# Kernel tuning notes

Hardware: AMD Instinct MI355X
Metric: run time of the kernel (lower is better)

## Reference

```python
import jax, jax.numpy as jnp
import numpy as np

N_NODES = 50000
IN_CH = 128
HID = 128
OUT_CH = 40
N_LAYERS = 3
N_EDGES = 600000


def setup_inputs() -> dict:
    key = jax.random.key(0)
    ks = jax.random.split(key, 4 + 5 * N_LAYERS)
    x = jax.random.normal(ks[0], (N_NODES, IN_CH), dtype=jnp.float32)
    edge_attr = jax.random.normal(ks[1], (N_EDGES, 4), dtype=jnp.float32)
    edge_index = jax.random.randint(ks[2], (2, N_EDGES), 0, N_NODES, dtype=jnp.int64)
    # Per-layer MLP params ([in->hid->hid]); in==hid so stack as [L, d, d].
    def glorot(k, fan_in, fan_out):
        s = jnp.sqrt(2.0 / (fan_in + fan_out)).astype(jnp.float32)
        return jax.random.normal(k, (fan_in, fan_out), dtype=jnp.float32) * s
    W1 = jnp.stack([glorot(ks[3 + i], IN_CH if i == 0 else HID, HID) for i in range(N_LAYERS)])
    b1 = jnp.zeros((N_LAYERS, HID), dtype=jnp.float32)
    W2 = jnp.stack([glorot(ks[3 + N_LAYERS + i], HID, HID) for i in range(N_LAYERS)])
    b2 = jnp.zeros((N_LAYERS, HID), dtype=jnp.float32)
    Wc = glorot(ks[3 + 2 * N_LAYERS], HID, OUT_CH)
    bc = jnp.zeros((OUT_CH,), dtype=jnp.float32)
    return {"x": x, "edge_attr": edge_attr, "edge_index": edge_index,
            "W1": W1, "b1": b1, "W2": W2, "b2": b2, "Wc": Wc, "bc": bc}


def reference(x, edge_attr, edge_index, W1, b1, W2, b2, Wc, bc):
    # GIN node classifier, eval mode (dropout = identity, BN = identity).
    src, dst = edge_index[0], edge_index[1]
    h = x
    for i in range(N_LAYERS):
        # GINConv (eps=0): aggregate sum of neighbor features via scatter-add.
        msgs = h[src]                                   # [E, d] gather
        aggr = jax.ops.segment_sum(msgs, dst, num_segments=N_NODES)  # [N, d]
        z = h + aggr                                    # (1+eps)*x + sum
        z = jax.nn.relu(z @ W1[i] + b1[i])              # MLP hidden
        z = z @ W2[i] + b2[i]                           # MLP out
        h = jax.nn.relu(z)                              # F.relu(conv(...))
    return h @ Wc + bc                                  # [N, OUT_CH]
```

## Files before the change

### kernel.cpp

```cpp
#include <hip/hip_runtime.h>

#define N_NODES 50000
#define IN_CH 128
#define HID 128
#define OUT_CH 40
#define N_LAYERS 3
#define N_EDGES 600000
#define DSTRIDE 64
#define DEGSTRIDE 32

typedef __attribute__((ext_vector_type(8))) short short8;
typedef __attribute__((ext_vector_type(4))) float floatx4;

static __device__ __forceinline__ unsigned short f32_to_bf16(float f) {
  unsigned u = __float_as_uint(f);
  unsigned r = 0x7FFFu + ((u >> 16) & 1u);
  return (unsigned short)((u + r) >> 16);
}
static __device__ __forceinline__ float bf16_to_f32(unsigned short h) {
  return __uint_as_float(((unsigned)h) << 16);
}

#define CONV_BLOCKS 6250
#define W_BLOCKS 408
#define DEG_BLOCKS 1563

__global__ __launch_bounds__(256) void prep_all_kernel(
    const float* __restrict__ x, const float* __restrict__ W1,
    const float* __restrict__ W2, const float* __restrict__ Wc,
    unsigned short* __restrict__ xb, unsigned short* __restrict__ WT,
    unsigned short* __restrict__ WcT, unsigned short* __restrict__ hb1,
    int* __restrict__ deg) {
  const int b = blockIdx.x;
  const int t = threadIdx.x;
  if (b < CONV_BLOCKS) {
    int i = (b * 256 + t) * 4;
    if (i < N_NODES * 128) {
      float4 v = *(const float4*)(x + i);
      ushort4 o;
      o.x = f32_to_bf16(v.x); o.y = f32_to_bf16(v.y);
      o.z = f32_to_bf16(v.z); o.w = f32_to_bf16(v.w);
      *(ushort4*)(xb + i) = o;
    }
  } else if (b < CONV_BLOCKS + W_BLOCKS) {
    int o = (b - CONV_BLOCKS) * 256 + t;
    if (o < 6 * 16384) {
      int mat = o >> 14;
      int r = o & 16383;
      int n = r >> 7;
      int k = r & 127;
      const float* W = (mat < 3) ? (W1 + (size_t)mat * 16384)
                                 : (W2 + (size_t)(mat - 3) * 16384);
      WT[(size_t)mat * 16384 + (size_t)n * 128 + k] =
          f32_to_bf16(W[(size_t)k * 128 + n]);
    } else if (o < 6 * 16384 + 48 * 128) {
      int r = o - 6 * 16384;
      int n = r >> 7;
      int k = r & 127;
      float v = (n < OUT_CH) ? Wc[(size_t)k * OUT_CH + n] : 0.0f;
      WcT[(size_t)n * 128 + k] = f32_to_bf16(v);
    }
  } else if (b < CONV_BLOCKS + W_BLOCKS + DEG_BLOCKS) {
    int i = ((b - CONV_BLOCKS - W_BLOCKS) * 256 + t) * 4;
    if (i < N_NODES * DEGSTRIDE) *(int4*)(deg + i) = make_int4(0, 0, 0, 0);
  } else {
    if (t < 128) xb[(size_t)N_NODES * 128 + t] = 0;
    else hb1[(size_t)N_NODES * 128 + (t - 128)] = 0;
  }
}

#define CSR_BLOCKS 586
__global__ __launch_bounds__(256) void csr_kernel(
    const int* __restrict__ ei, int* __restrict__ deg, int* __restrict__ col) {
  int base = (blockIdx.x * 256 + threadIdx.x) * 4;
  if (base >= N_EDGES) return;
  int4 s4 = *(const int4*)(ei + base);
  int4 d4 = *(const int4*)(ei + N_EDGES + base);
  int p0 = atomicAdd(&deg[(size_t)d4.x * DEGSTRIDE], 1);
  int p1 = atomicAdd(&deg[(size_t)d4.y * DEGSTRIDE], 1);
  int p2 = atomicAdd(&deg[(size_t)d4.z * DEGSTRIDE], 1);
  int p3 = atomicAdd(&deg[(size_t)d4.w * DEGSTRIDE], 1);
  col[(size_t)d4.x * DSTRIDE + p0] = s4.x;
  col[(size_t)d4.y * DSTRIDE + p1] = s4.y;
  col[(size_t)d4.z * DSTRIDE + p2] = s4.z;
  col[(size_t)d4.w * DSTRIDE + p3] = s4.w;
}

__global__ __launch_bounds__(256) void aggregate_kernel(
    const unsigned short* __restrict__ h, const int* __restrict__ deg,
    const int* __restrict__ col, unsigned short* __restrict__ z) {
  int n = __builtin_amdgcn_readfirstlane(blockIdx.x * 4 + (threadIdx.x >> 6));
  int q = threadIdx.x & 63;
  const size_t co = (size_t)q * 2;
  ushort2 sv = *(const ushort2*)(h + (size_t)n * 128 + co);
  float ax[8], ay[8];
#pragma unroll
  for (int k = 0; k < 8; ++k) { ax[k] = 0.f; ay[k] = 0.f; }
  ax[0] = bf16_to_f32(sv.x);
  ay[0] = bf16_to_f32(sv.y);
  int dg = __builtin_amdgcn_readfirstlane(deg[(size_t)n * DEGSTRIDE]);
  int cnt = (dg + 15) & ~15;
  const int* cp = col + (size_t)n * DSTRIDE;
  for (int i = 0; i < cnt; i += 16) {
    int ss[16];
#pragma unroll
    for (int k = 0; k < 16; ++k) {
      int sl = cp[i + k];
      ss[k] = __builtin_amdgcn_readfirstlane((i + k < dg) ? sl : N_NODES);
    }
    ushort2 vv[16];
#pragma unroll
    for (int k = 0; k < 16; ++k)
      vv[k] = *(const ushort2*)(h + (size_t)ss[k] * 128 + co);
#pragma unroll
    for (int k = 0; k < 16; ++k) {
      ax[k & 7] += bf16_to_f32(vv[k].x);
      ay[k & 7] += bf16_to_f32(vv[k].y);
    }
  }
  float s0 = (ax[0] + ax[1]) + (ax[2] + ax[3]) + (ax[4] + ax[5]) + (ax[6] + ax[7]);
  float s1 = (ay[0] + ay[1]) + (ay[2] + ay[3]) + (ay[4] + ay[5]) + (ay[6] + ay[7]);
  ushort2 o;
  o.x = f32_to_bf16(s0);
  o.y = f32_to_bf16(s1);
  *(ushort2*)(z + (size_t)n * 128 + co) = o;
}

template <bool LAST>
__global__ __launch_bounds__(256) void layer_pair_kernel(
    const unsigned short* __restrict__ A, const unsigned short* __restrict__ WT1,
    const float* __restrict__ b1, const unsigned short* __restrict__ WT2,
    const float* __restrict__ b2, unsigned short* __restrict__ Z,
    const unsigned short* __restrict__ WcT, const float* __restrict__ bc,
    float* __restrict__ out, int M) {
  __shared__ __align__(16) unsigned short Wl[128][136];
  __shared__ __align__(16) unsigned short T[64][136];
  const int tid = threadIdx.x;
  const int w = tid >> 6;
  const int lane = tid & 63;
  const int qg = lane >> 4;
  const int ln = lane & 15;
  const int row0 = blockIdx.x * 64;
  const int rbase = w * 16;
  const int r0 = row0 + rbase + ln;
  const short8 zero8 = {0, 0, 0, 0, 0, 0, 0, 0};

#pragma unroll
  for (int j = 0; j < 8; ++j) {
    int slot = tid + j * 256;
    int row = slot >> 4;
    int kb = slot & 15;
    *(short8*)&Wl[row][kb * 8] = *(const short8*)(WT1 + (size_t)row * 128 + kb * 8);
  }
  __syncthreads();

  floatx4 acc[8];
#pragma unroll
  for (int ct = 0; ct < 8; ++ct) acc[ct] = (floatx4){0.f, 0.f, 0.f, 0.f};
#pragma unroll
  for (int ks = 0; ks < 4; ++ks) {
    const int koff = ks * 32 + qg * 8;
    short8 a = (r0 < M) ? *(const short8*)(A + (size_t)r0 * 128 + koff) : zero8;
#pragma unroll
    for (int ct = 0; ct < 8; ++ct) {
      short8 b = *(const short8*)&Wl[ct * 16 + ln][koff];
      acc[ct] = __builtin_amdgcn_mfma_f32_16x16x32_bf16(a, b, acc[ct], 0, 0, 0);
    }
  }
#pragma unroll
  for (int ct = 0; ct < 8; ++ct) {
    float bv = b1[ct * 16 + ln];
#pragma unroll
    for (int r = 0; r < 4; ++r) {
      float v = fmaxf(acc[ct][r] + bv, 0.0f);
      T[rbase + qg * 4 + r][ct * 16 + ln] = f32_to_bf16(v);
    }
  }

  __syncthreads();
#pragma unroll
  for (int j = 0; j < 8; ++j) {
    int slot = tid + j * 256;
    int row = slot >> 4;
    int kb = slot & 15;
    *(short8*)&Wl[row][kb * 8] = *(const short8*)(WT2 + (size_t)row * 128 + kb * 8);
  }
  __syncthreads();

  floatx4 acc2[8];
#pragma unroll
  for (int ct = 0; ct < 8; ++ct) acc2[ct] = (floatx4){0.f, 0.f, 0.f, 0.f};
#pragma unroll
  for (int ks = 0; ks < 4; ++ks) {
    const int koff = ks * 32 + qg * 8;
    short8 a = *(const short8*)&T[rbase + ln][koff];
#pragma unroll
    for (int ct = 0; ct < 8; ++ct) {
      short8 b = *(const short8*)&Wl[ct * 16 + ln][koff];
      acc2[ct] = __builtin_amdgcn_mfma_f32_16x16x32_bf16(a, b, acc2[ct], 0, 0, 0);
    }
  }
#pragma unroll
  for (int ct = 0; ct < 8; ++ct) {
    float bv = b2[ct * 16 + ln];
#pragma unroll
    for (int r = 0; r < 4; ++r) {
      float v = fmaxf(acc2[ct][r] + bv, 0.0f);
      T[rbase + qg * 4 + r][ct * 16 + ln] = f32_to_bf16(v);
    }
  }

  if (LAST) {
    floatx4 acc3[3];
#pragma unroll
    for (int ct = 0; ct < 3; ++ct) acc3[ct] = (floatx4){0.f, 0.f, 0.f, 0.f};
#pragma unroll
    for (int ks = 0; ks < 4; ++ks) {
      const int koff = ks * 32 + qg * 8;
      short8 a = *(const short8*)&T[rbase + ln][koff];
#pragma unroll
      for (int ct = 0; ct < 3; ++ct) {
        short8 b = *(const short8*)(WcT + (size_t)(ct * 16 + ln) * 128 + koff);
        acc3[ct] = __builtin_amdgcn_mfma_f32_16x16x32_bf16(a, b, acc3[ct], 0, 0, 0);
      }
    }
#pragma unroll
    for (int ct = 0; ct < 3; ++ct) {
      int colg = ct * 16 + ln;
      if (colg < OUT_CH) {
        float bv = bc[colg];
#pragma unroll
        for (int r = 0; r < 4; ++r) {
          int row = row0 + rbase + qg * 4 + r;
          if (row < M) out[(size_t)row * OUT_CH + colg] = acc3[ct][r] + bv;
        }
      }
    }
  } else {
    __syncthreads();
#pragma unroll
    for (int j = 0; j < 4; ++j) {
      int slot = tid + j * 256;
      int row = slot >> 4;
      int kb = slot & 15;
      if (row0 + row < M) {
        short8 v = *(const short8*)&T[row][kb * 8];
        *(short8*)(Z + (size_t)(row0 + row) * 128 + kb * 8) = v;
      }
    }
  }
}

extern "C" void kernel_launch(void* const* d_in, const int* in_sizes, int n_in,
                              void* d_out, int out_size, void* d_ws,
                              size_t ws_size, hipStream_t stream) {
  const float* x = (const float*)d_in[0];
  const int* ei = (const int*)d_in[2];
  const float* W1 = (const float*)d_in[3];
  const float* b1 = (const float*)d_in[4];
  const float* W2 = (const float*)d_in[5];
  const float* b2 = (const float*)d_in[6];
  const float* Wc = (const float*)d_in[7];
  const float* bc = (const float*)d_in[8];
  float* out = (float*)d_out;

  const size_t NF = (size_t)(N_NODES + 1) * 128;
  unsigned short* hb0 = (unsigned short*)d_ws;
  unsigned short* hb1 = hb0 + NF;
  unsigned short* xbf = hb1 + NF;
  unsigned short* WT = xbf + NF;
  unsigned short* WcT = WT + 6 * 16384;
  int* deg = (int*)(WcT + 48 * 128);
  int* col = deg + (size_t)N_NODES * DEGSTRIDE;

  const dim3 blk(256);
  const int aggr_grid = N_NODES / 4;
  const int pair_grid = (N_NODES + 63) / 64;

  prep_all_kernel<<<CONV_BLOCKS + W_BLOCKS + DEG_BLOCKS + 1, blk, 0, stream>>>(
      x, W1, W2, Wc, xbf, WT, WcT, hb1, deg);

  csr_kernel<<<CSR_BLOCKS, blk, 0, stream>>>(ei, deg, col);

  const unsigned short* h = xbf;
  for (int l = 0; l < N_LAYERS; ++l) {
    aggregate_kernel<<<aggr_grid, blk, 0, stream>>>(h, deg, col, hb0);
    if (l < N_LAYERS - 1) {
      layer_pair_kernel<false><<<pair_grid, blk, 0, stream>>>(
          hb0, WT + (size_t)l * 16384, b1 + (size_t)l * 128,
          WT + (size_t)(3 + l) * 16384, b2 + (size_t)l * 128, hb1,
          nullptr, nullptr, nullptr, N_NODES);
      h = hb1;
    } else {
      layer_pair_kernel<true><<<pair_grid, blk, 0, stream>>>(
          hb0, WT + (size_t)l * 16384, b1 + (size_t)l * 128,
          WT + (size_t)(3 + l) * 16384, b2 + (size_t)l * 128, nullptr,
          WcT, bc, out, N_NODES);
    }
  }
}
```

Before: 245.5 us.

## Gather neighbor rows with 16-byte loads split across lane groups in aggregation

The aggregation kernel now has each wavefront split into four 16-lane groups. Each group loads a whole neighbor row with 16-byte short8 loads, handling four neighbors per step, and the partial sums are combined with cross-lane shuffles. Previously every lane did a 4-byte load per neighbor, so this cuts the number of memory instructions per gathered row at the cost of extra shuffles and idle lanes in the final store. The CSR build kernel also changes from four edges per thread with int4 loads to one edge per thread with a larger grid.

```diff
diff --git a/kernel.cpp b/kernel.cpp
--- a/kernel.cpp
+++ b/kernel.cpp
@@ -69,61 +69,61 @@
   }
 }
 
-#define CSR_BLOCKS 586
 __global__ __launch_bounds__(256) void csr_kernel(
     const int* __restrict__ ei, int* __restrict__ deg, int* __restrict__ col) {
-  int base = (blockIdx.x * 256 + threadIdx.x) * 4;
-  if (base >= N_EDGES) return;
-  int4 s4 = *(const int4*)(ei + base);
-  int4 d4 = *(const int4*)(ei + N_EDGES + base);
-  int p0 = atomicAdd(&deg[(size_t)d4.x * DEGSTRIDE], 1);
-  int p1 = atomicAdd(&deg[(size_t)d4.y * DEGSTRIDE], 1);
-  int p2 = atomicAdd(&deg[(size_t)d4.z * DEGSTRIDE], 1);
-  int p3 = atomicAdd(&deg[(size_t)d4.w * DEGSTRIDE], 1);
-  col[(size_t)d4.x * DSTRIDE + p0] = s4.x;
-  col[(size_t)d4.y * DSTRIDE + p1] = s4.y;
-  col[(size_t)d4.z * DSTRIDE + p2] = s4.z;
-  col[(size_t)d4.w * DSTRIDE + p3] = s4.w;
+  int e = blockIdx.x * 256 + threadIdx.x;
+  if (e >= N_EDGES) return;
+  int s = ei[e];
+  int d = ei[N_EDGES + e];
+  int pos = atomicAdd(&deg[(size_t)d * DEGSTRIDE], 1);
+  col[(size_t)d * DSTRIDE + pos] = s;
 }
 
 __global__ __launch_bounds__(256) void aggregate_kernel(
     const unsigned short* __restrict__ h, const int* __restrict__ deg,
     const int* __restrict__ col, unsigned short* __restrict__ z) {
   int n = __builtin_amdgcn_readfirstlane(blockIdx.x * 4 + (threadIdx.x >> 6));
-  int q = threadIdx.x & 63;
-  const size_t co = (size_t)q * 2;
-  ushort2 sv = *(const ushort2*)(h + (size_t)n * 128 + co);
-  float ax[8], ay[8];
-#pragma unroll
-  for (int k = 0; k < 8; ++k) { ax[k] = 0.f; ay[k] = 0.f; }
-  ax[0] = bf16_to_f32(sv.x);
-  ay[0] = bf16_to_f32(sv.y);
+  const int lane = threadIdx.x & 63;
+  const int g = lane >> 4;
+  const int p = lane & 15;
+  short8 sv = *(const short8*)(h + (size_t)n * 128 + p * 8);
+  float acc[8];
+#pragma unroll
+  for (int j = 0; j < 8; ++j)
+    acc[j] = (g == 0) ? bf16_to_f32((unsigned short)sv[j]) : 0.f;
+
   int dg = __builtin_amdgcn_readfirstlane(deg[(size_t)n * DEGSTRIDE]);
   int cnt = (dg + 15) & ~15;
   const int* cp = col + (size_t)n * DSTRIDE;
   for (int i = 0; i < cnt; i += 16) {
-    int ss[16];
-#pragma unroll
-    for (int k = 0; k < 16; ++k) {
-      int sl = cp[i + k];
-      ss[k] = __builtin_amdgcn_readfirstlane((i + k < dg) ? sl : N_NODES);
-    }
-    ushort2 vv[16];
-#pragma unroll
-    for (int k = 0; k < 16; ++k)
-      vv[k] = *(const ushort2*)(h + (size_t)ss[k] * 128 + co);
-#pragma unroll
-    for (int k = 0; k < 16; ++k) {
-      ax[k & 7] += bf16_to_f32(vv[k].x);
-      ay[k & 7] += bf16_to_f32(vv[k].y);
-    }
-  }
-  float s0 = (ax[0] + ax[1]) + (ax[2] + ax[3]) + (ax[4] + ax[5]) + (ax[6] + ax[7]);
-  float s1 = (ay[0] + ay[1]) + (ay[2] + ay[3]) + (ay[4] + ay[5]) + (ay[6] + ay[7]);
-  ushort2 o;
-  o.x = f32_to_bf16(s0);
-  o.y = f32_to_bf16(s1);
-  *(ushort2*)(z + (size_t)n * 128 + co) = o;
+    short8 v[4];
+#pragma unroll
+    for (int b = 0; b < 4; ++b) {
+      int r = i + b * 4;
+      int s0 = __builtin_amdgcn_readfirstlane((r + 0 < dg) ? cp[r + 0] : N_NODES);
+      int s1 = __builtin_amdgcn_readfirstlane((r + 1 < dg) ? cp[r + 1] : N_NODES);
+      int s2 = __builtin_amdgcn_readfirstlane((r + 2 < dg) ? cp[r + 2] : N_NODES);
+      int s3 = __builtin_amdgcn_readfirstlane((r + 3 < dg) ? cp[r + 3] : N_NODES);
+      int myrow = (g == 1) ? s1 : (g == 2) ? s2 : (g == 3) ? s3 : s0;
+      v[b] = *(const short8*)(h + (size_t)myrow * 128 + p * 8);
+    }
+#pragma unroll
+    for (int b = 0; b < 4; ++b)
+#pragma unroll
+      for (int j = 0; j < 8; ++j)
+        acc[j] += bf16_to_f32((unsigned short)v[b][j]);
+  }
+#pragma unroll
+  for (int j = 0; j < 8; ++j) {
+    acc[j] += __shfl_xor(acc[j], 16, 64);
+    acc[j] += __shfl_xor(acc[j], 32, 64);
+  }
+  if (g == 0) {
+    short8 o;
+#pragma unroll
+    for (int j = 0; j < 8; ++j) o[j] = (short)f32_to_bf16(acc[j]);
+    *(short8*)(z + (size_t)n * 128 + p * 8) = o;
+  }
 }
 
 template <bool LAST>
@@ -274,13 +274,14 @@
   int* col = deg + (size_t)N_NODES * DEGSTRIDE;
 
   const dim3 blk(256);
+  const int edge_grid = (N_EDGES + 255) / 256;
   const int aggr_grid = N_NODES / 4;
   const int pair_grid = (N_NODES + 63) / 64;
 
   prep_all_kernel<<<CONV_BLOCKS + W_BLOCKS + DEG_BLOCKS + 1, blk, 0, stream>>>(
       x, W1, W2, Wc, xbf, WT, WcT, hb1, deg);
 
-  csr_kernel<<<CSR_BLOCKS, blk, 0, stream>>>(ei, deg, col);
+  csr_kernel<<<edge_grid, blk, 0, stream>>>(ei, deg, col);
 
   const unsigned short* h = xbf;
   for (int l = 0; l < N_LAYERS; ++l) {
```

New measurement: 255.6 us. 4.1% more time.

## Replace padded per-node CSR with atomicExch linked lists for edge adjacency

Applied to the files above, without the earlier changes.

Builds per-destination adjacency as singly linked lists using atomicExch on a head array, and stores (src,next) pairs per edge instead of writing into fixed 64-slot padded rows. The aggregation kernel walks two node lists per wavefront in an interleaved loop, so each wave processes two nodes. This shrinks the adjacency memory and the zeroing work, and removes the degree cap of 64. The cost is a serial pointer-chasing dependency per edge, which replaces the previous 16-wide batched index loads and adds latency on every hop.

```diff
diff --git a/kernel.cpp b/kernel.cpp
--- a/kernel.cpp
+++ b/kernel.cpp
@@ -6,8 +6,7 @@
 #define OUT_CH 40
 #define N_LAYERS 3
 #define N_EDGES 600000
-#define DSTRIDE 64
-#define DEGSTRIDE 32
+#define HEADSTRIDE 16
 
 typedef __attribute__((ext_vector_type(8))) short short8;
 typedef __attribute__((ext_vector_type(4))) float floatx4;
@@ -23,14 +22,14 @@
 
 #define CONV_BLOCKS 6250
 #define W_BLOCKS 408
-#define DEG_BLOCKS 1563
+#define HEAD_BLOCKS 782
 
 __global__ __launch_bounds__(256) void prep_all_kernel(
     const float* __restrict__ x, const float* __restrict__ W1,
     const float* __restrict__ W2, const float* __restrict__ Wc,
     unsigned short* __restrict__ xb, unsigned short* __restrict__ WT,
     unsigned short* __restrict__ WcT, unsigned short* __restrict__ hb1,
-    int* __restrict__ deg) {
+    int* __restrict__ head) {
   const int b = blockIdx.x;
   const int t = threadIdx.x;
   if (b < CONV_BLOCKS) {
@@ -60,9 +59,10 @@
       float v = (n < OUT_CH) ? Wc[(size_t)k * OUT_CH + n] : 0.0f;
       WcT[(size_t)n * 128 + k] = f32_to_bf16(v);
     }
-  } else if (b < CONV_BLOCKS + W_BLOCKS + DEG_BLOCKS) {
+  } else if (b < CONV_BLOCKS + W_BLOCKS + HEAD_BLOCKS) {
     int i = ((b - CONV_BLOCKS - W_BLOCKS) * 256 + t) * 4;
-    if (i < N_NODES * DEGSTRIDE) *(int4*)(deg + i) = make_int4(0, 0, 0, 0);
+    if (i < N_NODES * HEADSTRIDE)
+      *(int4*)(head + i) = make_int4(-1, -1, -1, -1);
   } else {
     if (t < 128) xb[(size_t)N_NODES * 128 + t] = 0;
     else hb1[(size_t)N_NODES * 128 + (t - 128)] = 0;
@@ -71,59 +71,57 @@
 
 #define CSR_BLOCKS 586
 __global__ __launch_bounds__(256) void csr_kernel(
-    const int* __restrict__ ei, int* __restrict__ deg, int* __restrict__ col) {
+    const int* __restrict__ ei, int* __restrict__ head, int* __restrict__ lst) {
   int base = (blockIdx.x * 256 + threadIdx.x) * 4;
   if (base >= N_EDGES) return;
   int4 s4 = *(const int4*)(ei + base);
   int4 d4 = *(const int4*)(ei + N_EDGES + base);
-  int p0 = atomicAdd(&deg[(size_t)d4.x * DEGSTRIDE], 1);
-  int p1 = atomicAdd(&deg[(size_t)d4.y * DEGSTRIDE], 1);
-  int p2 = atomicAdd(&deg[(size_t)d4.z * DEGSTRIDE], 1);
-  int p3 = atomicAdd(&deg[(size_t)d4.w * DEGSTRIDE], 1);
-  col[(size_t)d4.x * DSTRIDE + p0] = s4.x;
-  col[(size_t)d4.y * DSTRIDE + p1] = s4.y;
-  col[(size_t)d4.z * DSTRIDE + p2] = s4.z;
-  col[(size_t)d4.w * DSTRIDE + p3] = s4.w;
+  int n0 = atomicExch(&head[(size_t)d4.x * HEADSTRIDE], base + 0);
+  int n1 = atomicExch(&head[(size_t)d4.y * HEADSTRIDE], base + 1);
+  int n2 = atomicExch(&head[(size_t)d4.z * HEADSTRIDE], base + 2);
+  int n3 = atomicExch(&head[(size_t)d4.w * HEADSTRIDE], base + 3);
+  *(int4*)(lst + 2 * (size_t)base) = make_int4(s4.x, n0, s4.y, n1);
+  *(int4*)(lst + 2 * (size_t)base + 4) = make_int4(s4.z, n2, s4.w, n3);
 }
 
 __global__ __launch_bounds__(256) void aggregate_kernel(
-    const unsigned short* __restrict__ h, const int* __restrict__ deg,
-    const int* __restrict__ col, unsigned short* __restrict__ z) {
-  int n = __builtin_amdgcn_readfirstlane(blockIdx.x * 4 + (threadIdx.x >> 6));
-  int q = threadIdx.x & 63;
+    const unsigned short* __restrict__ h, const int* __restrict__ head,
+    const int* __restrict__ lst, unsigned short* __restrict__ z) {
+  const int w = threadIdx.x >> 6;
+  int n0 = __builtin_amdgcn_readfirstlane(blockIdx.x * 8 + w * 2);
+  int n1 = n0 + 1;
+  const int q = threadIdx.x & 63;
   const size_t co = (size_t)q * 2;
-  ushort2 sv = *(const ushort2*)(h + (size_t)n * 128 + co);
-  float ax[8], ay[8];
-#pragma unroll
-  for (int k = 0; k < 8; ++k) { ax[k] = 0.f; ay[k] = 0.f; }
-  ax[0] = bf16_to_f32(sv.x);
-  ay[0] = bf16_to_f32(sv.y);
-  int dg = __builtin_amdgcn_readfirstlane(deg[(size_t)n * DEGSTRIDE]);
-  int cnt = (dg + 15) & ~15;
-  const int* cp = col + (size_t)n * DSTRIDE;
-  for (int i = 0; i < cnt; i += 16) {
-    int ss[16];
-#pragma unroll
-    for (int k = 0; k < 16; ++k) {
-      int sl = cp[i + k];
-      ss[k] = __builtin_amdgcn_readfirstlane((i + k < dg) ? sl : N_NODES);
-    }
-    ushort2 vv[16];
-#pragma unroll
-    for (int k = 0; k < 16; ++k)
-      vv[k] = *(const ushort2*)(h + (size_t)ss[k] * 128 + co);
-#pragma unroll
-    for (int k = 0; k < 16; ++k) {
-      ax[k & 7] += bf16_to_f32(vv[k].x);
-      ay[k & 7] += bf16_to_f32(vv[k].y);
-    }
-  }
-  float s0 = (ax[0] + ax[1]) + (ax[2] + ax[3]) + (ax[4] + ax[5]) + (ax[6] + ax[7]);
-  float s1 = (ay[0] + ay[1]) + (ay[2] + ay[3]) + (ay[4] + ay[5]) + (ay[6] + ay[7]);
-  ushort2 o;
-  o.x = f32_to_bf16(s0);
-  o.y = f32_to_bf16(s1);
-  *(ushort2*)(z + (size_t)n * 128 + co) = o;
+  ushort2 sv0 = *(const ushort2*)(h + (size_t)n0 * 128 + co);
+  ushort2 sv1 = *(const ushort2*)(h + (size_t)n1 * 128 + co);
+  float a0x = bf16_to_f32(sv0.x), a0y = bf16_to_f32(sv0.y);
+  float a1x = bf16_to_f32(sv1.x), a1y = bf16_to_f32(sv1.y);
+  int e0 = __builtin_amdgcn_readfirstlane(head[(size_t)n0 * HEADSTRIDE]);
+  int e1 = __builtin_amdgcn_readfirstlane(head[(size_t)n1 * HEADSTRIDE]);
+  while (e0 != -1 || e1 != -1) {
+    int s0 = N_NODES, nx0 = -1, s1 = N_NODES, nx1 = -1;
+    if (e0 != -1) {
+      int2 p = *(const int2*)(lst + 2 * (size_t)e0);
+      s0 = p.x; nx0 = p.y;
+    }
+    if (e1 != -1) {
+      int2 p = *(const int2*)(lst + 2 * (size_t)e1);
+      s1 = p.x; nx1 = p.y;
+    }
+    s0 = __builtin_amdgcn_readfirstlane(s0);
+    s1 = __builtin_amdgcn_readfirstlane(s1);
+    ushort2 v0 = *(const ushort2*)(h + (size_t)s0 * 128 + co);
+    ushort2 v1 = *(const ushort2*)(h + (size_t)s1 * 128 + co);
+    a0x += bf16_to_f32(v0.x); a0y += bf16_to_f32(v0.y);
+    a1x += bf16_to_f32(v1.x); a1y += bf16_to_f32(v1.y);
+    e0 = __builtin_amdgcn_readfirstlane(nx0);
+    e1 = __builtin_amdgcn_readfirstlane(nx1);
+  }
+  ushort2 o0, o1;
+  o0.x = f32_to_bf16(a0x); o0.y = f32_to_bf16(a0y);
+  o1.x = f32_to_bf16(a1x); o1.y = f32_to_bf16(a1y);
+  *(ushort2*)(z + (size_t)n0 * 128 + co) = o0;
+  *(ushort2*)(z + (size_t)n1 * 128 + co) = o1;
 }
 
 template <bool LAST>
@@ -270,21 +268,21 @@
   unsigned short* xbf = hb1 + NF;
   unsigned short* WT = xbf + NF;
   unsigned short* WcT = WT + 6 * 16384;
-  int* deg = (int*)(WcT + 48 * 128);
-  int* col = deg + (size_t)N_NODES * DEGSTRIDE;
+  int* head = (int*)(WcT + 48 * 128);
+  int* lst = head + (size_t)N_NODES * HEADSTRIDE;
 
   const dim3 blk(256);
-  const int aggr_grid = N_NODES / 4;
+  const int aggr_grid = N_NODES / 8;
   const int pair_grid = (N_NODES + 63) / 64;
 
-  prep_all_kernel<<<CONV_BLOCKS + W_BLOCKS + DEG_BLOCKS + 1, blk, 0, stream>>>(
-      x, W1, W2, Wc, xbf, WT, WcT, hb1, deg);
-
-  csr_kernel<<<CSR_BLOCKS, blk, 0, stream>>>(ei, deg, col);
+  prep_all_kernel<<<CONV_BLOCKS + W_BLOCKS + HEAD_BLOCKS + 1, blk, 0, stream>>>(
+      x, W1, W2, Wc, xbf, WT, WcT, hb1, head);
+
+  csr_kernel<<<CSR_BLOCKS, blk, 0, stream>>>(ei, head, lst);
 
   const unsigned short* h = xbf;
   for (int l = 0; l < N_LAYERS; ++l) {
-    aggregate_kernel<<<aggr_grid, blk, 0, stream>>>(h, deg, col, hb0);
+    aggregate_kernel<<<aggr_grid, blk, 0, stream>>>(h, head, lst, hb0);
     if (l < N_LAYERS - 1) {
       layer_pair_kernel<false><<<pair_grid, blk, 0, stream>>>(
           hb0, WT + (size_t)l * 16384, b1 + (size_t)l * 128,
```

Result: slower. 332.0 us (+35.3%).

## Fuse neighbor aggregation into per-layer MLP kernel via shared-memory tile

Applied to the files above, without the earlier changes.

Moves the gather-sum aggregation into the layer MLP kernel: each wave aggregates its 16 nodes directly into the LDS tile T, which then feeds the first MFMA GEMM. This removes three aggregate launches and the global round trip of the aggregated features. In exchange, aggregation parallelism drops from 12500 blocks with one node per wave to 782 blocks with 16 serial nodes per wave, which may expose gather latency and lower occupancy. The CSR build is also changed to one edge per thread, and both hidden buffers now get a zero padding row.

```diff
diff --git a/kernel.cpp b/kernel.cpp
--- a/kernel.cpp
+++ b/kernel.cpp
@@ -29,8 +29,8 @@
     const float* __restrict__ x, const float* __restrict__ W1,
     const float* __restrict__ W2, const float* __restrict__ Wc,
     unsigned short* __restrict__ xb, unsigned short* __restrict__ WT,
-    unsigned short* __restrict__ WcT, unsigned short* __restrict__ hb1,
-    int* __restrict__ deg) {
+    unsigned short* __restrict__ WcT, unsigned short* __restrict__ hb0,
+    unsigned short* __restrict__ hb1, int* __restrict__ deg) {
   const int b = blockIdx.x;
   const int t = threadIdx.x;
   if (b < CONV_BLOCKS) {
@@ -64,75 +64,33 @@
     int i = ((b - CONV_BLOCKS - W_BLOCKS) * 256 + t) * 4;
     if (i < N_NODES * DEGSTRIDE) *(int4*)(deg + i) = make_int4(0, 0, 0, 0);
   } else {
-    if (t < 128) xb[(size_t)N_NODES * 128 + t] = 0;
-    else hb1[(size_t)N_NODES * 128 + (t - 128)] = 0;
-  }
-}
-
-#define CSR_BLOCKS 586
+    if (t < 128) {
+      xb[(size_t)N_NODES * 128 + t] = 0;
+      hb0[(size_t)N_NODES * 128 + t] = 0;
+    } else {
+      hb1[(size_t)N_NODES * 128 + (t - 128)] = 0;
+    }
+  }
+}
+
 __global__ __launch_bounds__(256) void csr_kernel(
     const int* __restrict__ ei, int* __restrict__ deg, int* __restrict__ col) {
-  int base = (blockIdx.x * 256 + threadIdx.x) * 4;
-  if (base >= N_EDGES) return;
-  int4 s4 = *(const int4*)(ei + base);
-  int4 d4 = *(const int4*)(ei + N_EDGES + base);
-  int p0 = atomicAdd(&deg[(size_t)d4.x * DEGSTRIDE], 1);
-  int p1 = atomicAdd(&deg[(size_t)d4.y * DEGSTRIDE], 1);
-  int p2 = atomicAdd(&deg[(size_t)d4.z * DEGSTRIDE], 1);
-  int p3 = atomicAdd(&deg[(size_t)d4.w * DEGSTRIDE], 1);
-  col[(size_t)d4.x * DSTRIDE + p0] = s4.x;
-  col[(size_t)d4.y * DSTRIDE + p1] = s4.y;
-  col[(size_t)d4.z * DSTRIDE + p2] = s4.z;
-  col[(size_t)d4.w * DSTRIDE + p3] = s4.w;
-}
-
-__global__ __launch_bounds__(256) void aggregate_kernel(
+  int e = blockIdx.x * 256 + threadIdx.x;
+  if (e >= N_EDGES) return;
+  int s = ei[e];
+  int d = ei[N_EDGES + e];
+  int pos = atomicAdd(&deg[(size_t)d * DEGSTRIDE], 1);
+  col[(size_t)d * DSTRIDE + pos] = s;
+}
+
+template <bool LAST>
+__global__ __launch_bounds__(256) void fused_layer_kernel(
     const unsigned short* __restrict__ h, const int* __restrict__ deg,
-    const int* __restrict__ col, unsigned short* __restrict__ z) {
-  int n = __builtin_amdgcn_readfirstlane(blockIdx.x * 4 + (threadIdx.x >> 6));
-  int q = threadIdx.x & 63;
-  const size_t co = (size_t)q * 2;
-  ushort2 sv = *(const ushort2*)(h + (size_t)n * 128 + co);
-  float ax[8], ay[8];
-#pragma unroll
-  for (int k = 0; k < 8; ++k) { ax[k] = 0.f; ay[k] = 0.f; }
-  ax[0] = bf16_to_f32(sv.x);
-  ay[0] = bf16_to_f32(sv.y);
-  int dg = __builtin_amdgcn_readfirstlane(deg[(size_t)n * DEGSTRIDE]);
-  int cnt = (dg + 15) & ~15;
-  const int* cp = col + (size_t)n * DSTRIDE;
-  for (int i = 0; i < cnt; i += 16) {
-    int ss[16];
-#pragma unroll
-    for (int k = 0; k < 16; ++k) {
-      int sl = cp[i + k];
-      ss[k] = __builtin_amdgcn_readfirstlane((i + k < dg) ? sl : N_NODES);
-    }
-    ushort2 vv[16];
-#pragma unroll
-    for (int k = 0; k < 16; ++k)
-      vv[k] = *(const ushort2*)(h + (size_t)ss[k] * 128 + co);
-#pragma unroll
-    for (int k = 0; k < 16; ++k) {
-      ax[k & 7] += bf16_to_f32(vv[k].x);
-      ay[k & 7] += bf16_to_f32(vv[k].y);
-    }
-  }
-  float s0 = (ax[0] + ax[1]) + (ax[2] + ax[3]) + (ax[4] + ax[5]) + (ax[6] + ax[7]);
-  float s1 = (ay[0] + ay[1]) + (ay[2] + ay[3]) + (ay[4] + ay[5]) + (ay[6] + ay[7]);
-  ushort2 o;
-  o.x = f32_to_bf16(s0);
-  o.y = f32_to_bf16(s1);
-  *(ushort2*)(z + (size_t)n * 128 + co) = o;
-}
-
-template <bool LAST>
-__global__ __launch_bounds__(256) void layer_pair_kernel(
-    const unsigned short* __restrict__ A, const unsigned short* __restrict__ WT1,
+    const int* __restrict__ col, const unsigned short* __restrict__ WT1,
     const float* __restrict__ b1, const unsigned short* __restrict__ WT2,
     const float* __restrict__ b2, unsigned short* __restrict__ Z,
     const unsigned short* __restrict__ WcT, const float* __restrict__ bc,
-    float* __restrict__ out, int M) {
+    float* __restrict__ out) {
   __shared__ __align__(16) unsigned short Wl[128][136];
   __shared__ __align__(16) unsigned short T[64][136];
   const int tid = threadIdx.x;
@@ -142,8 +100,6 @@
   const int ln = lane & 15;
   const int row0 = blockIdx.x * 64;
   const int rbase = w * 16;
-  const int r0 = row0 + rbase + ln;
-  const short8 zero8 = {0, 0, 0, 0, 0, 0, 0, 0};
 
 #pragma unroll
   for (int j = 0; j < 8; ++j) {
@@ -152,6 +108,46 @@
     int kb = slot & 15;
     *(short8*)&Wl[row][kb * 8] = *(const short8*)(WT1 + (size_t)row * 128 + kb * 8);
   }
+
+  const size_t co = (size_t)lane * 2;
+  for (int idx = 0; idx < 16; ++idx) {
+    int nid = row0 + rbase + idx;
+    int hn = (nid < N_NODES) ? nid : N_NODES;
+    ushort2 sv = *(const ushort2*)(h + (size_t)hn * 128 + co);
+    float ax[8], ay[8];
+#pragma unroll
+    for (int k = 0; k < 8; ++k) { ax[k] = 0.f; ay[k] = 0.f; }
+    ax[0] = bf16_to_f32(sv.x);
+    ay[0] = bf16_to_f32(sv.y);
+    int dg = 0;
+    if (nid < N_NODES)
+      dg = __builtin_amdgcn_readfirstlane(deg[(size_t)nid * DEGSTRIDE]);
+    int cnt = (dg + 15) & ~15;
+    const int* cp = col + (size_t)nid * DSTRIDE;
+    for (int i = 0; i < cnt; i += 16) {
+      int ss[16];
+#pragma unroll
+      for (int k = 0; k < 16; ++k) {
+        int sl = cp[i + k];
+        ss[k] = __builtin_amdgcn_readfirstlane((i + k < dg) ? sl : N_NODES);
+      }
+      ushort2 vv[16];
+#pragma unroll
+      for (int k = 0; k < 16; ++k)
+        vv[k] = *(const ushort2*)(h + (size_t)ss[k] * 128 + co);
+#pragma unroll
+      for (int k = 0; k < 16; ++k) {
+        ax[k & 7] += bf16_to_f32(vv[k].x);
+        ay[k & 7] += bf16_to_f32(vv[k].y);
+      }
+    }
+    float s0 = (ax[0] + ax[1]) + (ax[2] + ax[3]) + (ax[4] + ax[5]) + (ax[6] + ax[7]);
+    float s1 = (ay[0] + ay[1]) + (ay[2] + ay[3]) + (ay[4] + ay[5]) + (ay[6] + ay[7]);
+    ushort2 o;
+    o.x = f32_to_bf16(s0);
+    o.y = f32_to_bf16(s1);
+    *(ushort2*)&T[rbase + idx][lane * 2] = o;
+  }
   __syncthreads();
 
   floatx4 acc[8];
@@ -160,7 +156,7 @@
 #pragma unroll
   for (int ks = 0; ks < 4; ++ks) {
     const int koff = ks * 32 + qg * 8;
-    short8 a = (r0 < M) ? *(const short8*)(A + (size_t)r0 * 128 + koff) : zero8;
+    short8 a = *(const short8*)&T[rbase + ln][koff];
 #pragma unroll
     for (int ct = 0; ct < 8; ++ct) {
       short8 b = *(const short8*)&Wl[ct * 16 + ln][koff];
@@ -232,7 +228,7 @@
 #pragma unroll
         for (int r = 0; r < 4; ++r) {
           int row = row0 + rbase + qg * 4 + r;
-          if (row < M) out[(size_t)row * OUT_CH + colg] = acc3[ct][r] + bv;
+          if (row < N_NODES) out[(size_t)row * OUT_CH + colg] = acc3[ct][r] + bv;
         }
       }
     }
@@ -243,7 +239,7 @@
       int slot = tid + j * 256;
       int row = slot >> 4;
       int kb = slot & 15;
-      if (row0 + row < M) {
+      if (row0 + row < N_NODES) {
         short8 v = *(const short8*)&T[row][kb * 8];
         *(short8*)(Z + (size_t)(row0 + row) * 128 + kb * 8) = v;
       }
@@ -274,28 +270,21 @@
   int* col = deg + (size_t)N_NODES * DEGSTRIDE;
 
   const dim3 blk(256);
-  const int aggr_grid = N_NODES / 4;
-  const int pair_grid = (N_NODES + 63) / 64;
+  const int edge_grid = (N_EDGES + 255) / 256;
+  const int layer_grid = (N_NODES + 63) / 64;
 
   prep_all_kernel<<<CONV_BLOCKS + W_BLOCKS + DEG_BLOCKS + 1, blk, 0, stream>>>(
-      x, W1, W2, Wc, xbf, WT, WcT, hb1, deg);
-
-  csr_kernel<<<CSR_BLOCKS, blk, 0, stream>>>(ei, deg, col);
-
-  const unsigned short* h = xbf;
-  for (int l = 0; l < N_LAYERS; ++l) {
-    aggregate_kernel<<<aggr_grid, blk, 0, stream>>>(h, deg, col, hb0);
-    if (l < N_LAYERS - 1) {
-      layer_pair_kernel<false><<<pair_grid, blk, 0, stream>>>(
-          hb0, WT + (size_t)l * 16384, b1 + (size_t)l * 128,
-          WT + (size_t)(3 + l) * 16384, b2 + (size_t)l * 128, hb1,
-          nullptr, nullptr, nullptr, N_NODES);
-      h = hb1;
-    } else {
-      layer_pair_kernel<true><<<pair_grid, blk, 0, stream>>>(
-          hb0, WT + (size_t)l * 16384, b1 + (size_t)l * 128,
-          WT + (size_t)(3 + l) * 16384, b2 + (size_t)l * 128, nullptr,
-          WcT, bc, out, N_NODES);
-    }
-  }
-}
+      x, W1, W2, Wc, xbf, WT, WcT, hb0, hb1, deg);
+
+  csr_kernel<<<edge_grid, blk, 0, stream>>>(ei, deg, col);
+
+  fused_layer_kernel<false><<<layer_grid, blk, 0, stream>>>(
+      xbf, deg, col, WT + 0 * 16384, b1 + 0 * 128, WT + 3 * 16384, b2 + 0 * 128,
+      hb0, nullptr, nullptr, nullptr);
+  fused_layer_kernel<false><<<layer_grid, blk, 0, stream>>>(
+      hb0, deg, col, WT + 1 * 16384, b1 + 1 * 128, WT + 4 * 16384, b2 + 1 * 128,
+      hb1, nullptr, nullptr, nullptr);
+  fused_layer_kernel<true><<<layer_grid, blk, 0, stream>>>(
+      hb1, deg, col, WT + 2 * 16384, b1 + 2 * 128, WT + 5 * 16384, b2 + 2 * 128,
+      nullptr, WcT, bc, out);
+}
```

After: 313.2 us. 1.28x slower.
